# Optimization experiments

Measured on AMD Instinct MI355X. Metric: run time of the kernel, lower is better.

## Reference

```python
import jax, jax.numpy as jnp
import numpy as np

N_HEADS = 16
NEG = -1000000000.0  # masked_fill value from the original code


def setup_inputs() -> dict:
    key = jax.random.key(0)
    ks = jax.random.split(key, 7)
    D = 1024
    x = jax.random.normal(ks[0], (2, 2048, D), dtype=jnp.float32)
    s = 1.0 / np.sqrt(D)
    Wq = jax.random.normal(ks[1], (D, D), dtype=jnp.float32) * s
    bq = jax.random.normal(ks[2], (D,), dtype=jnp.float32) * 0.01
    Wk = jax.random.normal(ks[3], (D, D), dtype=jnp.float32) * s
    bk = jax.random.normal(ks[4], (D,), dtype=jnp.float32) * 0.01
    Wv = jax.random.normal(ks[5], (D, D), dtype=jnp.float32) * s
    bv = jax.random.normal(ks[6], (D,), dtype=jnp.float32) * 0.01
    return {"x": x, "Wq": Wq, "bq": bq, "Wk": Wk, "bk": bk, "Wv": Wv, "bv": bv}


def reference(x, Wq, bq, Wk, bk, Wv, bv):
    B, S, D = x.shape
    H = N_HEADS
    dh = D // H
    # nn.Linear: x @ W.T + b
    Q = (x @ Wq.T + bq).reshape(B, S, H, dh)
    K = (x @ Wk.T + bk).reshape(B, S, H, dh)
    V = (x @ Wv.T + bv).reshape(B, S, H, dh)
    # NOTE: original scales by sqrt(n_heads), not sqrt(d_head) -- faithful.
    scale = jnp.asarray(H, x.dtype) ** 0.5
    scores = jnp.einsum('bqhd,bkhd->bhqk', Q, K) / scale  # [B,H,S,S]
    # Original: mask = triu(ones, diag=1); scores.masked_fill(mask == 0, -1e9)
    # i.e. positions where the STRICT-UPPER mask is False (lower triangle incl.
    # diagonal) get -1e9. Faithful reproduction of that (buggy) behavior.
    triu = jnp.triu(jnp.ones((S, S), dtype=bool), k=1)  # [S,S]
    scores = jnp.where(triu[None, None, :, :], scores, jnp.asarray(NEG, x.dtype))
    probs = jax.nn.softmax(scores, axis=-1)
    # dropout is identity at inference
    out = jnp.einsum('bhqk,bkhd->bqhd', probs, V).reshape(B, S, D)
    return out
```

## Files before the change

kernel.cpp:

```cpp
#include <hip/hip_runtime.h>
#include <stdint.h>

typedef unsigned short u16;
typedef __attribute__((ext_vector_type(8))) short bf16x8;
typedef __attribute__((ext_vector_type(4))) float floatx4;
typedef __attribute__((ext_vector_type(16))) float floatx16;
typedef __attribute__((ext_vector_type(4))) unsigned uintx4;

#define MFMA16(a, b, c) __builtin_amdgcn_mfma_f32_16x16x32_bf16(a, b, c, 0, 0, 0)
#define MFMA32(a, b, c) __builtin_amdgcn_mfma_f32_32x32x16_bf16(a, b, c, 0, 0, 0)
#define MEMFENCE asm volatile("" ::: "memory")

#if __has_builtin(__builtin_amdgcn_exp2f)
#define EXP2(x) __builtin_amdgcn_exp2f(x)
#else
#define EXP2(x) __expf(0.6931471805599453f * (x))
#endif

__device__ __forceinline__ u16 f2bf(float f) {
  unsigned u = __builtin_bit_cast(unsigned, f);
  return (u16)((u + 0x7FFFu + ((u >> 16) & 1u)) >> 16);
}
__device__ __forceinline__ unsigned pkbf(float a, float b) {
  unsigned ua = __builtin_bit_cast(unsigned, a);
  unsigned ub = __builtin_bit_cast(unsigned, b);
  return ((ua + 0x8000u) >> 16) | ((ub + 0x8000u) & 0xFFFF0000u);
}
__device__ __forceinline__ float bf2f(u16 v) {
  return __builtin_bit_cast(float, (unsigned)v << 16);
}

__device__ __forceinline__ void glds16(void* lds, const void* g) {
  __builtin_amdgcn_global_load_lds((const __attribute__((address_space(1))) void*)g,
                                   (__attribute__((address_space(3))) void*)lds,
                                   16, 0, 0);
}


__global__ __launch_bounds__(256) void cvt_all(
    const float* __restrict__ x, const float* __restrict__ w0,
    const float* __restrict__ w1, const float* __restrict__ w2,
    u16* __restrict__ xb, u16* __restrict__ Wb) {
  const int bid = blockIdx.x;
  const float* src;
  u16* dst;
  int i;
  if (bid < 4096) {
    src = x; dst = xb; i = bid * 256 + threadIdx.x;
  } else {
    const int z = (bid - 4096) >> 10;
    src = (z == 0) ? w0 : (z == 1) ? w1 : w2;
    dst = Wb + (size_t)z * (1024 * 1024);
    i = ((bid - 4096) & 1023) * 256 + threadIdx.x;
  }
  float4 f = reinterpret_cast<const float4*>(src)[i];
  ushort4 o;
  o.x = f2bf(f.x); o.y = f2bf(f.y); o.z = f2bf(f.z); o.w = f2bf(f.w);
  reinterpret_cast<ushort4*>(dst)[i] = o;
}

__global__ __launch_bounds__(256, 3) void qkv_gemm(
    const u16* __restrict__ xb, const u16* __restrict__ Wb,
    const float* __restrict__ bq, const float* __restrict__ bk,
    const float* __restrict__ bv,
    u16* __restrict__ Qb, u16* __restrict__ Kb, u16* __restrict__ VTb) {
  __shared__ __attribute__((aligned(16))) u16 smem[2 * 128 * 64];
  u16* As = smem;
  u16* Bs = smem + 128 * 64;

  const int tid = threadIdx.x;
  const int w = tid >> 6, lane = tid & 63;
  const int lo = lane & 15, quad = lane >> 4;
  const int which = blockIdx.z;
  const int m0 = blockIdx.x * 128, n0 = blockIdx.y * 128;

  const u16* W = Wb + (size_t)which * (1024 * 1024);
  const int wm = (w >> 1) * 64, wn = (w & 1) * 64;

  floatx4 acc[4][4];
  for (int i = 0; i < 4; ++i)
    for (int j = 0; j < 4; ++j) acc[i][j] = (floatx4)0.f;

  const int arow = lane >> 3;
  const int aswz = ((lane & 7) ^ arow) * 8;

  for (int kt = 0; kt < 16; ++kt) {
    const int k0 = kt * 64;
    for (int j = 0; j < 4; ++j) {
      const int seg = w * 4 + j;
      glds16(As + seg * 512, xb + (size_t)(m0 + seg * 8 + arow) * 1024 + k0 + aswz);
      glds16(Bs + seg * 512, W + (size_t)(n0 + seg * 8 + arow) * 1024 + k0 + aswz);
    }
    __syncthreads();
    for (int kk = 0; kk < 2; ++kk) {
      const int swz = ((kk * 4 + quad) ^ (lo & 7)) * 8;
      bf16x8 af[4], bfr[4];
      for (int it = 0; it < 4; ++it)
        af[it] = *reinterpret_cast<const bf16x8*>(As + (wm + it * 16 + lo) * 64 + swz);
      for (int jt = 0; jt < 4; ++jt)
        bfr[jt] = *reinterpret_cast<const bf16x8*>(Bs + (wn + jt * 16 + lo) * 64 + swz);
      for (int it = 0; it < 4; ++it)
        for (int jt = 0; jt < 4; ++jt)
          acc[it][jt] = MFMA16(af[it], bfr[jt], acc[it][jt]);
    }
    __syncthreads();
  }

  const float* bias = (which == 0) ? bq : (which == 1) ? bk : bv;
  float bb[4];
  for (int jt = 0; jt < 4; ++jt) bb[jt] = bias[n0 + wn + jt * 16 + lo];
  const int b = m0 >> 11;

  if (which < 2) {
    const float scl = (which == 0) ? 0.36067376022224085f : 1.0f;
    u16* Tw = smem + w * (16 * 72);
    const int hblk = (n0 + wn) >> 6;
    const int bh = b * 16 + hblk;
    u16* dstQ = Qb + ((size_t)bh * 2048 + ((m0 & 2047) + wm)) * 64;
    u16* dstK = Kb + (size_t)bh * 131072;
    for (int it = 0; it < 4; ++it) {
      for (int jt = 0; jt < 4; ++jt)
        for (int r = 0; r < 4; ++r) {
          const int m = quad * 4 + r, col = jt * 16 + lo;
          Tw[m * 72 + (((col >> 3) ^ (m & 7)) * 8) + (col & 7)] =
              f2bf((acc[it][jt][r] + bb[jt]) * scl);
        }
      MEMFENCE;
      for (int rd = 0; rd < 2; ++rd) {
        const int sr = rd * 8 + (lane >> 3), d8 = lane & 7;
        bf16x8 v = *reinterpret_cast<const bf16x8*>(Tw + sr * 72 + ((d8 ^ (sr & 7)) * 8));
        if (which == 0) {
          *reinterpret_cast<bf16x8*>(dstQ + (size_t)(it * 16 + sr) * 64 + d8 * 8) = v;
        } else {
          const int s = (m0 & 2047) + wm + it * 16 + sr;
          const size_t idx = (size_t)(s >> 6) * 4096 + (d8 >> 1) * 1024 +
                             ((s >> 5) & 1) * 512 + (d8 & 1) * 256 + (s & 31) * 8;
          *reinterpret_cast<bf16x8*>(dstK + idx) = v;
        }
      }
      MEMFENCE;
    }
  } else {
    for (int pass = 0; pass < 2; ++pass) {
      if ((wm >> 6) == pass) {
        for (int it = 0; it < 4; ++it)
          for (int jt = 0; jt < 4; ++jt)
            for (int r = 0; r < 4; ++r) {
              const int n = wn + jt * 16 + lo;
              const int m = it * 16 + quad * 4 + r;
              smem[n * 72 + (((m >> 3) ^ (n & 7)) * 8) + (m & 7)] =
                  f2bf(acc[it][jt][r] + bb[jt]);
            }
      }
      __syncthreads();
      for (int rd = 0; rd < 4; ++rd) {
        const int n = (tid >> 3) + rd * 32, m8 = tid & 7;
        bf16x8 v = *reinterpret_cast<const bf16x8*>(smem + n * 72 + ((m8 ^ (n & 7)) * 8));
        const int ng = n0 + n, hh = ng >> 6, dloc = ng & 63;
        const int s0 = (m0 & 2047) + pass * 64 + m8 * 8;
        const size_t idx = (size_t)(s0 >> 6) * 4096 + ((s0 >> 4) & 3) * 1024 +
                           (dloc >> 5) * 512 + ((s0 >> 3) & 1) * 256 + (dloc & 31) * 8;
        *reinterpret_cast<bf16x8*>(VTb + (size_t)(b * 16 + hh) * 131072 + idx) = v;
      }
      __syncthreads();
    }
  }
}

__global__ __launch_bounds__(64, 2) void attn(
    const u16* __restrict__ Qb, const u16* __restrict__ Kb,
    const u16* __restrict__ VTb, float* __restrict__ out) {
  const int L = blockIdx.x;
  const int bh = L & 31;
  const int qt = L >> 5;
  const int kstart = qt >> 1;
  const int n = 32 - kstart;

  const int lane = threadIdx.x & 63;
  const int l31 = lane & 31, h = lane >> 5;

  const u16* Qh = Qb + (size_t)bh * (2048 * 64);
  const u16* Kf = Kb + (size_t)bh * 131072;
  const u16* Vf = VTb + (size_t)bh * 131072;

  const int qrow = qt * 32 + l31;
  bf16x8 qf[4];
  for (int kk = 0; kk < 4; ++kk)
    qf[kk] = *reinterpret_cast<const bf16x8*>(Qh + (size_t)qrow * 64 + kk * 16 + h * 8);

  float lrun = 0.f;
  floatx16 acc[2];
  acc[0] = (floatx16)0.f;
  acc[1] = (floatx16)0.f;

#define LOADK(D, kt_)                                                         \
  _Pragma("unroll") for (int ci = 0; ci < 8; ++ci)                            \
      D[ci] = *reinterpret_cast<const bf16x8*>(                               \
          Kf + (size_t)((kt_) * 8 + ci) * 512 + lane * 8);
#define LOADV(D, kt_)                                                         \
  _Pragma("unroll") for (int ci = 0; ci < 8; ++ci)                            \
      D[ci] = *reinterpret_cast<const bf16x8*>(                               \
          Vf + (size_t)((kt_) * 8 + ci) * 512 + lane * 8);

#define ITER(KC, VC, KN, VN)                                                  \
  {                                                                           \
    const int kt = kstart + i;                                                \
    floatx16 sc[2];                                                           \
    sc[0] = (floatx16)0.f;                                                    \
    sc[1] = (floatx16)0.f;                                                    \
    _Pragma("unroll") for (int kk = 0; kk < 4; ++kk)                          \
      _Pragma("unroll") for (int m = 0; m < 2; ++m)                           \
          sc[m] = MFMA32(KC[kk * 2 + m], qf[kk], sc[m]);                      \
    if (i + 1 < n) { LOADK(KN, kt + 1); LOADV(VN, kt + 1); }                  \
    const bool maskp = (i == 0);                                              \
    unsigned pw[2][8];                                                        \
    _Pragma("unroll") for (int m = 0; m < 2; ++m)                             \
      _Pragma("unroll") for (int g = 0; g < 4; ++g) {                         \
        float p0 = EXP2(sc[m][4 * g + 0]), p1 = EXP2(sc[m][4 * g + 1]);       \
        float p2 = EXP2(sc[m][4 * g + 2]), p3 = EXP2(sc[m][4 * g + 3]);       \
        if (maskp) {                   \
          const int keyb = kt * 64 + m * 32 + 8 * g + 4 * h;                  \
          p0 = (keyb + 0 > qrow) ? p0 : 0.f;                                  \
          p1 = (keyb + 1 > qrow) ? p1 : 0.f;                                  \
          p2 = (keyb + 2 > qrow) ? p2 : 0.f;                                  \
          p3 = (keyb + 3 > qrow) ? p3 : 0.f;                                  \
        }                                                                     \
        lrun += (p0 + p1) + (p2 + p3);                                        \
        pw[m][2 * g] = pkbf(p0, p1);                                          \
        pw[m][2 * g + 1] = pkbf(p2, p3);                                      \
      }                                                                       \
    unsigned y[2][4];                                                         \
    _Pragma("unroll") for (int m = 0; m < 2; ++m)                             \
      _Pragma("unroll") for (int lh = 0; lh < 2; ++lh)                        \
        _Pragma("unroll") for (int j = 0; j < 2; ++j) {                       \
          const unsigned sv = h ? pw[m][4 * lh + j] : pw[m][4 * lh + 2 + j];  \
          y[m][2 * lh + j] = __shfl_xor(sv, 32);                              \
        }                                                                     \
    bf16x8 pb[4];                                                             \
    _Pragma("unroll") for (int c = 0; c < 4; ++c) {                           \
      const int m = c >> 1, lh = c & 1;                                       \
      uintx4 u;                                                               \
      u.x = h ? y[m][2 * lh]      : pw[m][4 * lh];                            \
      u.y = h ? y[m][2 * lh + 1]  : pw[m][4 * lh + 1];                        \
      u.z = h ? pw[m][4 * lh + 2] : y[m][2 * lh];                             \
      u.w = h ? pw[m][4 * lh + 3] : y[m][2 * lh + 1];                         \
      pb[c] = __builtin_bit_cast(bf16x8, u);                                  \
    }                                                                         \
    _Pragma("unroll") for (int c = 0; c < 4; ++c)                             \
      _Pragma("unroll") for (int dt = 0; dt < 2; ++dt)                        \
          acc[dt] = MFMA32(VC[c * 2 + dt], pb[c], acc[dt]);                   \
    ++i;                                                                      \
  }

  bf16x8 kA[8], vA[8], kB[8], vB[8];
  LOADK(kA, kstart);
  LOADV(vA, kstart);
  int i = 0;
  while (true) {
    ITER(kA, vA, kB, vB);
    if (i >= n) break;
    ITER(kB, vB, kA, vA);
    if (i >= n) break;
  }
#undef ITER
#undef LOADK
#undef LOADV

  lrun += __shfl_xor(lrun, 32);
  if (lrun != 0.f) {
    const float rl = 1.f / lrun;
    const int b = bh >> 4, hh = bh & 15;
    float* op = out + ((size_t)(b * 2048 + qrow)) * 1024 + hh * 64;
    for (int dt = 0; dt < 2; ++dt)
      for (int g = 0; g < 4; ++g) {
        float4 o4;
        o4.x = acc[dt][4 * g + 0] * rl;
        o4.y = acc[dt][4 * g + 1] * rl;
        o4.z = acc[dt][4 * g + 2] * rl;
        o4.w = acc[dt][4 * g + 3] * rl;
        *reinterpret_cast<float4*>(op + dt * 32 + 8 * g + 4 * h) = o4;
      }
  }
}

__global__ __launch_bounds__(256) void fix2047(const u16* __restrict__ VTb,
                                               float* __restrict__ out) {
  const int bh = blockIdx.x;
  const u16* Vh = VTb + (size_t)bh * 131072;
  const int t = threadIdx.x;
  const int d = t >> 2, j = t & 3;
  const int dt = d >> 5, l31 = d & 31;
  float s = 0.f;
  for (int kt = j * 8; kt < j * 8 + 8; ++kt)
    for (int c = 0; c < 4; ++c)
      for (int h = 0; h < 2; ++h) {
        bf16x8 v = *reinterpret_cast<const bf16x8*>(
            Vh + (size_t)kt * 4096 + c * 1024 + dt * 512 + h * 256 + l31 * 8);
        for (int e = 0; e < 8; ++e) s += bf2f((u16)v[e]);
      }
  s += __shfl_xor(s, 1);
  s += __shfl_xor(s, 2);
  if (j == 0) {
    const int b = bh >> 4, h = bh & 15;
    out[((size_t)(b * 2048 + 2047)) * 1024 + h * 64 + d] = s * (1.f / 2048.f);
  }
}

extern "C" void kernel_launch(void* const* d_in, const int* in_sizes, int n_in,
                              void* d_out, int out_size, void* d_ws, size_t ws_size,
                              hipStream_t stream) {
  const float* x  = (const float*)d_in[0];
  const float* Wq = (const float*)d_in[1];
  const float* bq = (const float*)d_in[2];
  const float* Wk = (const float*)d_in[3];
  const float* bk = (const float*)d_in[4];
  const float* Wv = (const float*)d_in[5];
  const float* bv = (const float*)d_in[6];
  float* out = (float*)d_out;

  char* ws = (char*)d_ws;
  u16* xb  = (u16*)(ws);
  u16* Wb  = (u16*)(ws + (8u << 20));
  u16* Qb  = (u16*)(ws + (14u << 20));
  u16* Kb  = (u16*)(ws + (22u << 20));
  u16* VTb = (u16*)(ws + (30u << 20));

  cvt_all<<<7168, 256, 0, stream>>>(x, Wq, Wk, Wv, xb, Wb);
  qkv_gemm<<<dim3(32, 8, 3), 256, 0, stream>>>(xb, Wb, bq, bk, bv, Qb, Kb, VTb);
  attn<<<dim3(2048), 64, 0, stream>>>(Qb, Kb, VTb, out);
  fix2047<<<dim3(32), 256, 0, stream>>>(VTb, out);
}
```

Baseline: 165.8 us.

## Pair complementary query tiles per block and stop prefetching V tiles

Each attention block now handles two query tiles, j and 63-j, in sequence. Because the key range is triangular, this gives every block roughly the same total work, and the grid is halved to 1024 blocks. V is no longer double-buffered. It is loaded for the current key tile inside each iteration, while only K is prefetched, which lowers register pressure. The trade-off is fewer concurrent blocks and V load latency that is now exposed on the critical path before the PV MFMAs.

```diff
diff --git a/kernel.cpp b/kernel.cpp
--- a/kernel.cpp
+++ b/kernel.cpp
@@ -172,9 +172,7 @@
     const u16* __restrict__ VTb, float* __restrict__ out) {
   const int L = blockIdx.x;
   const int bh = L & 31;
-  const int qt = L >> 5;
-  const int kstart = qt >> 1;
-  const int n = 32 - kstart;
+  const int j = L >> 5;
 
   const int lane = threadIdx.x & 63;
   const int l31 = lane & 31, h = lane >> 5;
@@ -182,16 +180,7 @@
   const u16* Qh = Qb + (size_t)bh * (2048 * 64);
   const u16* Kf = Kb + (size_t)bh * 131072;
   const u16* Vf = VTb + (size_t)bh * 131072;
-
-  const int qrow = qt * 32 + l31;
-  bf16x8 qf[4];
-  for (int kk = 0; kk < 4; ++kk)
-    qf[kk] = *reinterpret_cast<const bf16x8*>(Qh + (size_t)qrow * 64 + kk * 16 + h * 8);
-
-  float lrun = 0.f;
-  floatx16 acc[2];
-  acc[0] = (floatx16)0.f;
-  acc[1] = (floatx16)0.f;
+  const int b = bh >> 4, hh = bh & 15;
 
 #define LOADK(D, kt_)                                                         \
   _Pragma("unroll") for (int ci = 0; ci < 8; ++ci)                            \
@@ -202,7 +191,7 @@
       D[ci] = *reinterpret_cast<const bf16x8*>(                               \
           Vf + (size_t)((kt_) * 8 + ci) * 512 + lane * 8);
 
-#define ITER(KC, VC, KN, VN)                                                  \
+#define ITER(KC, KN)                                                          \
   {                                                                           \
     const int kt = kstart + i;                                                \
     floatx16 sc[2];                                                           \
@@ -211,7 +200,9 @@
     _Pragma("unroll") for (int kk = 0; kk < 4; ++kk)                          \
       _Pragma("unroll") for (int m = 0; m < 2; ++m)                           \
           sc[m] = MFMA32(KC[kk * 2 + m], qf[kk], sc[m]);                      \
-    if (i + 1 < n) { LOADK(KN, kt + 1); LOADV(VN, kt + 1); }                  \
+    bf16x8 vcur[8];                                                           \
+    LOADV(vcur, kt);                             \
+    if (i + 1 < n) { LOADK(KN, kt + 1); }                                     \
     const bool maskp = (i == 0);                                              \
     unsigned pw[2][8];                                                        \
     _Pragma("unroll") for (int m = 0; m < 2; ++m)                             \
@@ -232,11 +223,10 @@
     unsigned y[2][4];                                                         \
     _Pragma("unroll") for (int m = 0; m < 2; ++m)                             \
       _Pragma("unroll") for (int lh = 0; lh < 2; ++lh)                        \
-        _Pragma("unroll") for (int j = 0; j < 2; ++j) {                       \
-          const unsigned sv = h ? pw[m][4 * lh + j] : pw[m][4 * lh + 2 + j];  \
-          y[m][2 * lh + j] = __shfl_xor(sv, 32);                              \
+        _Pragma("unroll") for (int jj = 0; jj < 2; ++jj) {                    \
+          const unsigned sv = h ? pw[m][4 * lh + jj] : pw[m][4 * lh + 2 + jj];\
+          y[m][2 * lh + jj] = __shfl_xor(sv, 32);                             \
         }                                                                     \
-    bf16x8 pb[4];                                                             \
     _Pragma("unroll") for (int c = 0; c < 4; ++c) {                           \
       const int m = c >> 1, lh = c & 1;                                       \
       uintx4 u;                                                               \
@@ -244,43 +234,56 @@
       u.y = h ? y[m][2 * lh + 1]  : pw[m][4 * lh + 1];                        \
       u.z = h ? pw[m][4 * lh + 2] : y[m][2 * lh];                             \
       u.w = h ? pw[m][4 * lh + 3] : y[m][2 * lh + 1];                         \
-      pb[c] = __builtin_bit_cast(bf16x8, u);                                  \
+      bf16x8 pb = __builtin_bit_cast(bf16x8, u);                              \
+      acc[0] = MFMA32(vcur[c * 2 + 0], pb, acc[0]);                           \
+      acc[1] = MFMA32(vcur[c * 2 + 1], pb, acc[1]);                           \
     }                                                                         \
-    _Pragma("unroll") for (int c = 0; c < 4; ++c)                             \
-      _Pragma("unroll") for (int dt = 0; dt < 2; ++dt)                        \
-          acc[dt] = MFMA32(VC[c * 2 + dt], pb[c], acc[dt]);                   \
     ++i;                                                                      \
   }
 
-  bf16x8 kA[8], vA[8], kB[8], vB[8];
-  LOADK(kA, kstart);
-  LOADV(vA, kstart);
-  int i = 0;
-  while (true) {
-    ITER(kA, vA, kB, vB);
-    if (i >= n) break;
-    ITER(kB, vB, kA, vA);
-    if (i >= n) break;
+  for (int p = 0; p < 2; ++p) {
+    const int qt = (p == 0) ? j : 63 - j;
+    const int kstart = qt >> 1;
+    const int n = 32 - kstart;
+
+    const int qrow = qt * 32 + l31;
+    bf16x8 qf[4];
+    for (int kk = 0; kk < 4; ++kk)
+      qf[kk] = *reinterpret_cast<const bf16x8*>(Qh + (size_t)qrow * 64 + kk * 16 + h * 8);
+
+    float lrun = 0.f;
+    floatx16 acc[2];
+    acc[0] = (floatx16)0.f;
+    acc[1] = (floatx16)0.f;
+
+    bf16x8 kA[8], kB[8];
+    LOADK(kA, kstart);
+    int i = 0;
+    while (true) {
+      ITER(kA, kB);
+      if (i >= n) break;
+      ITER(kB, kA);
+      if (i >= n) break;
+    }
+
+    lrun += __shfl_xor(lrun, 32);
+    if (lrun != 0.f) {
+      const float rl = 1.f / lrun;
+      float* op = out + ((size_t)(b * 2048 + qrow)) * 1024 + hh * 64;
+      for (int dt = 0; dt < 2; ++dt)
+        for (int g = 0; g < 4; ++g) {
+          float4 o4;
+          o4.x = acc[dt][4 * g + 0] * rl;
+          o4.y = acc[dt][4 * g + 1] * rl;
+          o4.z = acc[dt][4 * g + 2] * rl;
+          o4.w = acc[dt][4 * g + 3] * rl;
+          *reinterpret_cast<float4*>(op + dt * 32 + 8 * g + 4 * h) = o4;
+        }
+    }
   }
 #undef ITER
 #undef LOADK
 #undef LOADV
-
-  lrun += __shfl_xor(lrun, 32);
-  if (lrun != 0.f) {
-    const float rl = 1.f / lrun;
-    const int b = bh >> 4, hh = bh & 15;
-    float* op = out + ((size_t)(b * 2048 + qrow)) * 1024 + hh * 64;
-    for (int dt = 0; dt < 2; ++dt)
-      for (int g = 0; g < 4; ++g) {
-        float4 o4;
-        o4.x = acc[dt][4 * g + 0] * rl;
-        o4.y = acc[dt][4 * g + 1] * rl;
-        o4.z = acc[dt][4 * g + 2] * rl;
-        o4.w = acc[dt][4 * g + 3] * rl;
-        *reinterpret_cast<float4*>(op + dt * 32 + 8 * g + 4 * h) = o4;
-      }
-  }
 }
 
 __global__ __launch_bounds__(256) void fix2047(const u16* __restrict__ VTb,
@@ -327,6 +330,6 @@
 
   cvt_all<<<7168, 256, 0, stream>>>(x, Wq, Wk, Wv, xb, Wb);
   qkv_gemm<<<dim3(32, 8, 3), 256, 0, stream>>>(xb, Wb, bq, bk, bv, Qb, Kb, VTb);
-  attn<<<dim3(2048), 64, 0, stream>>>(Qb, Kb, VTb, out);
+  attn<<<dim3(1024), 64, 0, stream>>>(Qb, Kb, VTb, out);
   fix2047<<<dim3(32), 256, 0, stream>>>(VTb, out);
 }
```

After: 164.6 us. About the same (-0.7%).
